# Kernel tuning notes

Hardware: AMD Instinct MI355X
Metric: run time of the kernel (lower is better)

Reference implementation:

```python
import jax, jax.numpy as jnp
import numpy as np

DIM = 384
NUM_HEADS = 12
KERNEL = 3
DILATIONS = (1, 2, 3)
B, H, W = 16, 56, 56


def _unfold(x, k, dil):
    # x: [B, c, H, W] -> [B, c, k*k, H, W]; matches nn.Unfold(k, dilation=dil,
    # padding=dil*(k-1)//2, stride=1) channel ordering [c, kh, kw].
    b, c, h, w = x.shape
    p = dil * (k - 1) // 2
    xp = jnp.pad(x, ((0, 0), (0, 0), (p, p), (p, p)))
    patches = [xp[:, :, i * dil:i * dil + h, j * dil:j * dil + w]
               for i in range(k) for j in range(k)]
    return jnp.stack(patches, axis=2)


def _dilate_attention(q, k, v, head_dim, kernel, dil):
    # q,k,v: [B, c, H, W]
    b, c, h, w = q.shape
    g = c // head_dim           # heads in this dilation branch
    kk = kernel * kernel
    scale = head_dim ** (-0.5)
    qg = q.reshape(b, g, head_dim, h * w)                       # [b,g,d,n]
    ku = _unfold(k, kernel, dil).reshape(b, g, head_dim, kk, h * w)
    vu = _unfold(v, kernel, dil).reshape(b, g, head_dim, kk, h * w)
    attn = jnp.einsum('bgdn,bgdkn->bgnk', qg, ku) * scale       # [b,g,n,kk]
    attn = jax.nn.softmax(attn, axis=-1)
    out = jnp.einsum('bgnk,bgdkn->bgnd', attn, vu)              # [b,g,n,d]
    return out.transpose(0, 2, 1, 3).reshape(b, h, w, c)        # [b,h,w,c]


def setup_inputs() -> dict:
    key = jax.random.key(0)
    kx, kq, kp = jax.random.split(key, 3)
    x = jax.random.normal(kx, (B, H, W, DIM), dtype=jnp.float32)
    w_qkv = jax.random.normal(kq, (3 * DIM, DIM), dtype=jnp.float32) * 0.02
    w_proj = jax.random.normal(kp, (DIM, DIM), dtype=jnp.float32) * 0.02
    b_proj = jnp.zeros((DIM,), dtype=jnp.float32)
    return {"x": x, "w_qkv": w_qkv, "w_proj": w_proj, "b_proj": b_proj}


def reference(x, w_qkv, w_proj, b_proj):
    b, h, w, c = x.shape
    nd = len(DILATIONS)
    cg = c // nd                # channels per dilation branch
    hd = c // NUM_HEADS         # head_dim
    xc = x.transpose(0, 3, 1, 2)                                 # [b,c,h,w]
    qkv = jnp.einsum('bchw,oc->bohw', xc, w_qkv)                 # 1x1 conv, no bias
    qkv = qkv.reshape(b, 3, nd, cg, h, w)
    outs = [_dilate_attention(qkv[:, 0, i], qkv[:, 1, i], qkv[:, 2, i],
                              hd, KERNEL, DILATIONS[i]) for i in range(nd)]
    y = jnp.stack(outs, axis=3).reshape(b, h, w, c)              # [b,h,w, nd*cg]
    return jnp.einsum('bhwc,oc->bhwo', y, w_proj) + b_proj
```

## Files before the change

### kernel.cpp

```cpp
#include <hip/hip_runtime.h>
#include <hip/hip_bf16.h>


#define NTOK 50176
#define ROWQKV 1152
#define CDIM 384

typedef _Float16 half2v __attribute__((ext_vector_type(2)));
typedef _Float16 half8 __attribute__((ext_vector_type(8)));
typedef float floatx4 __attribute__((ext_vector_type(4)));

typedef __attribute__((address_space(1))) const unsigned int GU32;
typedef __attribute__((address_space(3))) unsigned int LU32;

__global__ __launch_bounds__(256) void conv_f32_f16(const float* __restrict__ in,
                                                    _Float16* __restrict__ out, int n4) {
  int i = blockIdx.x * 256 + threadIdx.x;
  const int stride = gridDim.x * 256;
  for (; i < n4; i += stride) {
    float4 v = ((const float4*)in)[i];
    union { _Float16 h[4]; uint2 u; } o;
    o.h[0] = (_Float16)v.x; o.h[1] = (_Float16)v.y;
    o.h[2] = (_Float16)v.z; o.h[3] = (_Float16)v.w;
    ((uint2*)out)[i] = o.u;
  }
}

template <bool HALF_OUT>
__global__ __launch_bounds__(256) void gemm_f16(const _Float16* __restrict__ A,
                                                const _Float16* __restrict__ B,
                                                const float* __restrict__ bias,
                                                void* __restrict__ Cout,
                                                int N, int K) {
  __shared__ _Float16 As[128 * 32];
  __shared__ _Float16 Bs[128 * 32];
  const int tid = threadIdx.x;
  const int lane = tid & 63;
  const int wv = tid >> 6;
  const int wr = wv >> 1, wc = wv & 1;
  const size_t row0 = (size_t)blockIdx.x * 128;
  const int col0 = blockIdx.y * 128;

  const int srow = tid >> 2;
  const int sslot = tid & 3;
  const int gslot = sslot ^ ((srow >> 1) & 3);
  const _Float16* Abase = A + (row0 + srow) * (size_t)K + gslot * 8;
  const _Float16* Bbase = B + ((size_t)(col0 + srow)) * (size_t)K + gslot * 8;
  char* AsB = (char*)As;
  char* BsB = (char*)Bs;

  const int fr = lane & 15;
  const int fq = lane >> 4;
  const int rpos = (fq ^ ((fr >> 1) & 3)) * 8;

  floatx4 acc[4][4];
#pragma unroll
  for (int i = 0; i < 4; ++i)
#pragma unroll
    for (int j = 0; j < 4; ++j) acc[i][j] = (floatx4){0.f, 0.f, 0.f, 0.f};

  for (int k0 = 0; k0 < K; k0 += 32) {
    __builtin_amdgcn_global_load_lds((GU32*)(Abase + k0), (LU32*)(AsB + tid * 16), 16, 0, 0);
    __builtin_amdgcn_global_load_lds((GU32*)(Abase + (size_t)64 * K + k0),
                                     (LU32*)(AsB + tid * 16 + 4096), 16, 0, 0);
    __builtin_amdgcn_global_load_lds((GU32*)(Bbase + k0), (LU32*)(BsB + tid * 16), 16, 0, 0);
    __builtin_amdgcn_global_load_lds((GU32*)(Bbase + (size_t)64 * K + k0),
                                     (LU32*)(BsB + tid * 16 + 4096), 16, 0, 0);
    __syncthreads();
    half8 af[4], bf[4];
#pragma unroll
    for (int f = 0; f < 4; ++f) {
      af[f] = *(const half8*)&As[(wr * 64 + f * 16 + fr) * 32 + rpos];
      bf[f] = *(const half8*)&Bs[(wc * 64 + f * 16 + fr) * 32 + rpos];
    }
#pragma unroll
    for (int i = 0; i < 4; ++i)
#pragma unroll
      for (int j = 0; j < 4; ++j)
        acc[i][j] = __builtin_amdgcn_mfma_f32_16x16x32_f16(af[i], bf[j], acc[i][j], 0, 0, 0);
    __syncthreads();
  }

  const int crow = wr * 64 + (lane >> 4) * 4;
  const int ccol = wc * 64 + (lane & 15);
#pragma unroll
  for (int fm = 0; fm < 4; ++fm) {
#pragma unroll
    for (int fn = 0; fn < 4; ++fn) {
      const size_t r0 = (row0 + crow + fm * 16) * (size_t)N + col0 + ccol + fn * 16;
      if (HALF_OUT) {
        _Float16* C = (_Float16*)Cout;
#pragma unroll
        for (int j = 0; j < 4; ++j) C[r0 + (size_t)j * N] = (_Float16)acc[fm][fn][j];
      } else {
        float* C = (float*)Cout;
        const float bz = bias[col0 + ccol + fn * 16];
#pragma unroll
        for (int j = 0; j < 4; ++j) C[r0 + (size_t)j * N] = acc[fm][fn][j] + bz;
      }
    }
  }
}

__global__ __launch_bounds__(256) void attn_kernel(const _Float16* __restrict__ qkv,
                                                   _Float16* __restrict__ y) {
  const int idx = blockIdx.x * 256 + threadIdx.x;
  const int head = idx % 12;
  const int token = idx / 12;
  const int branch = head >> 2;
  const int dil = branch + 1;
  const int cbase = branch * 128 + (head & 3) * 32;
  const int xx = token % 56;
  const int yy = (token / 56) % 56;
  const int bimg = token / 3136;
  const float scale = 0.17677669529663687f;

  const _Float16* qp = qkv + (size_t)token * ROWQKV + cbase;
  half2v qh[16];
  *(half8*)&qh[0] = *(const half8*)(qp);
  *(half8*)&qh[4] = *(const half8*)(qp + 8);
  *(half8*)&qh[8] = *(const half8*)(qp + 16);
  *(half8*)&qh[12] = *(const half8*)(qp + 24);

  const size_t nbase = (size_t)bimg * 3136;

  float l[9];
#pragma unroll
  for (int j = 0; j < 9; ++j) {
    const int ny = yy + (j / 3 - 1) * dil;
    const int nx = xx + (j % 3 - 1) * dil;
    float d = 0.f;
    if ((unsigned)ny < 56u && (unsigned)nx < 56u) {
      const _Float16* kp = qkv + (nbase + ny * 56 + nx) * ROWQKV + 384 + cbase;
      half2v kh[16];
      *(half8*)&kh[0] = *(const half8*)(kp);
      *(half8*)&kh[4] = *(const half8*)(kp + 8);
      *(half8*)&kh[8] = *(const half8*)(kp + 16);
      *(half8*)&kh[12] = *(const half8*)(kp + 24);
#if __has_builtin(__builtin_amdgcn_fdot2)
#pragma unroll
      for (int c = 0; c < 16; ++c) d = __builtin_amdgcn_fdot2(qh[c], kh[c], d, false);
#else
#pragma unroll
      for (int c = 0; c < 16; ++c)
        d += (float)qh[c][0] * (float)kh[c][0] + (float)qh[c][1] * (float)kh[c][1];
#endif
    }
    l[j] = d * scale;
  }

  float m = l[0];
#pragma unroll
  for (int j = 1; j < 9; ++j) m = fmaxf(m, l[j]);
  float s = 0.f;
#pragma unroll
  for (int j = 0; j < 9; ++j) { l[j] = expf(l[j] - m); s += l[j]; }
  const float rs = 1.f / s;

  float out[32];
#pragma unroll
  for (int c = 0; c < 32; ++c) out[c] = 0.f;
#pragma unroll
  for (int j = 0; j < 9; ++j) {
    const int ny = yy + (j / 3 - 1) * dil;
    const int nx = xx + (j % 3 - 1) * dil;
    if ((unsigned)ny < 56u && (unsigned)nx < 56u) {
      const _Float16* vp = qkv + (nbase + ny * 56 + nx) * ROWQKV + 768 + cbase;
      half8 vh[4];
      vh[0] = *(const half8*)(vp);
      vh[1] = *(const half8*)(vp + 8);
      vh[2] = *(const half8*)(vp + 16);
      vh[3] = *(const half8*)(vp + 24);
      const float p = l[j];
#pragma unroll
      for (int g = 0; g < 4; ++g)
#pragma unroll
        for (int e = 0; e < 8; ++e) out[g * 8 + e] = fmaf(p, (float)vh[g][e], out[g * 8 + e]);
    }
  }

  _Float16* yp = y + (size_t)token * CDIM + cbase;
  half8 oh[4];
#pragma unroll
  for (int g = 0; g < 4; ++g) {
#pragma unroll
    for (int e = 0; e < 8; ++e) oh[g][e] = (_Float16)(out[g * 8 + e] * rs);
    *(half8*)(yp + g * 8) = oh[g];
  }
}

extern "C" void kernel_launch(void* const* d_in, const int* in_sizes, int n_in,
                              void* d_out, int out_size, void* d_ws, size_t ws_size,
                              hipStream_t stream) {
  const float* x = (const float*)d_in[0];
  const float* w_qkv = (const float*)d_in[1];
  const float* w_proj = (const float*)d_in[2];
  const float* b_proj = (const float*)d_in[3];
  float* out = (float*)d_out;

  _Float16* xh = (_Float16*)d_ws;
  _Float16* wqh = xh + (size_t)NTOK * CDIM;
  _Float16* wph = wqh + (size_t)ROWQKV * CDIM;
  _Float16* qkvh = wph + (size_t)CDIM * CDIM;
  _Float16* yh = qkvh + (size_t)NTOK * ROWQKV;

  conv_f32_f16<<<2048, 256, 0, stream>>>(x, xh, NTOK * CDIM / 4);
  conv_f32_f16<<<64, 256, 0, stream>>>(w_qkv, wqh, ROWQKV * CDIM / 4);
  conv_f32_f16<<<64, 256, 0, stream>>>(w_proj, wph, CDIM * CDIM / 4);

  gemm_f16<true><<<dim3(NTOK / 128, ROWQKV / 128), 256, 0, stream>>>(
      xh, wqh, nullptr, qkvh, ROWQKV, CDIM);

  attn_kernel<<<(NTOK * 12) / 256, 256, 0, stream>>>(qkvh, yh);

  gemm_f16<false><<<dim3(NTOK / 128, CDIM / 128), 256, 0, stream>>>(
      yh, wph, b_proj, out, CDIM, CDIM);
}
```

Measured before the change: 208.8 us.

## Fuse x fp32-to-fp16 conversion into QKV GEMM and double-buffer LDS tiles

The QKV GEMM now reads fp32 activations directly, converts them to fp16 in registers and writes them swizzled into LDS. This removes the separate conversion kernel and its fp16 copy of x. Both GEMMs also gain double-buffered LDS tiles, so the next K-slice is prefetched while MFMAs run on the current one, with one barrier per iteration instead of two. The cost is twice the LDS footprint, which may lower occupancy, and fp32 A is re-read once per column block (9 times for QKV), doubling A traffic compared with fp16.

```diff
diff --git a/kernel.cpp b/kernel.cpp
--- a/kernel.cpp
+++ b/kernel.cpp
@@ -26,28 +26,76 @@
   }
 }
 
-template <bool HALF_OUT>
-__global__ __launch_bounds__(256) void gemm_f16(const _Float16* __restrict__ A,
-                                                const _Float16* __restrict__ B,
-                                                const float* __restrict__ bias,
-                                                void* __restrict__ Cout,
-                                                int N, int K) {
-  __shared__ _Float16 As[128 * 32];
-  __shared__ _Float16 Bs[128 * 32];
+template <bool CONV_A, bool HALF_OUT>
+__global__ __launch_bounds__(256) void gemm2(const void* __restrict__ Aptr,
+                                             const _Float16* __restrict__ B,
+                                             const float* __restrict__ bias,
+                                             void* __restrict__ Cout,
+                                             int N, int K) {
+  __shared__ _Float16 As[2][128 * 32];
+  __shared__ _Float16 Bs[2][128 * 32];
   const int tid = threadIdx.x;
   const int lane = tid & 63;
   const int wv = tid >> 6;
   const int wr = wv >> 1, wc = wv & 1;
   const size_t row0 = (size_t)blockIdx.x * 128;
   const int col0 = blockIdx.y * 128;
+  const int NT = K / 32;
 
   const int srow = tid >> 2;
-  const int sslot = tid & 3;
-  const int gslot = sslot ^ ((srow >> 1) & 3);
-  const _Float16* Abase = A + (row0 + srow) * (size_t)K + gslot * 8;
+  const int gslot = (tid & 3) ^ ((srow >> 1) & 3);
   const _Float16* Bbase = B + ((size_t)(col0 + srow)) * (size_t)K + gslot * 8;
+  char* BsB = (char*)Bs;
+
+  const int ar = tid >> 1, ah = tid & 1;
+  const float* Af32 = (const float*)Aptr + (row0 + ar) * (size_t)K + ah * 16;
+  const int asw0 = (ah * 2) ^ ((ar >> 1) & 3);
+  const int asw1 = (ah * 2 + 1) ^ ((ar >> 1) & 3);
+  const _Float16* Abase16 = (const _Float16*)Aptr + (row0 + srow) * (size_t)K + gslot * 8;
   char* AsB = (char*)As;
-  char* BsB = (char*)Bs;
+
+  float4 av[4];
+  auto loadA = [&](int k0) {
+    if constexpr (CONV_A) {
+      av[0] = *(const float4*)(Af32 + k0);
+      av[1] = *(const float4*)(Af32 + k0 + 4);
+      av[2] = *(const float4*)(Af32 + k0 + 8);
+      av[3] = *(const float4*)(Af32 + k0 + 12);
+    } else {
+      __builtin_amdgcn_global_load_lds((GU32*)(Abase16 + k0), (LU32*)(AsB + tid * 16), 16, 0, 0);
+      __builtin_amdgcn_global_load_lds((GU32*)(Abase16 + (size_t)64 * K + k0),
+                                       (LU32*)(AsB + tid * 16 + 4096), 16, 0, 0);
+    }
+  };
+  auto loadA2 = [&](int k0, int buf) {
+    if constexpr (!CONV_A) {
+      __builtin_amdgcn_global_load_lds((GU32*)(Abase16 + k0),
+                                       (LU32*)(AsB + buf * 8192 + tid * 16), 16, 0, 0);
+      __builtin_amdgcn_global_load_lds((GU32*)(Abase16 + (size_t)64 * K + k0),
+                                       (LU32*)(AsB + buf * 8192 + tid * 16 + 4096), 16, 0, 0);
+    }
+  };
+  auto writeA = [&](int buf) {
+    if constexpr (CONV_A) {
+      half8 lo, hi;
+      lo[0] = (_Float16)av[0].x; lo[1] = (_Float16)av[0].y;
+      lo[2] = (_Float16)av[0].z; lo[3] = (_Float16)av[0].w;
+      lo[4] = (_Float16)av[1].x; lo[5] = (_Float16)av[1].y;
+      lo[6] = (_Float16)av[1].z; lo[7] = (_Float16)av[1].w;
+      hi[0] = (_Float16)av[2].x; hi[1] = (_Float16)av[2].y;
+      hi[2] = (_Float16)av[2].z; hi[3] = (_Float16)av[2].w;
+      hi[4] = (_Float16)av[3].x; hi[5] = (_Float16)av[3].y;
+      hi[6] = (_Float16)av[3].z; hi[7] = (_Float16)av[3].w;
+      *(half8*)&As[buf][ar * 32 + asw0 * 8] = lo;
+      *(half8*)&As[buf][ar * 32 + asw1 * 8] = hi;
+    }
+  };
+  auto stageB = [&](int k0, int buf) {
+    __builtin_amdgcn_global_load_lds((GU32*)(Bbase + k0),
+                                     (LU32*)(BsB + buf * 8192 + tid * 16), 16, 0, 0);
+    __builtin_amdgcn_global_load_lds((GU32*)(Bbase + (size_t)64 * K + k0),
+                                     (LU32*)(BsB + buf * 8192 + tid * 16 + 4096), 16, 0, 0);
+  };
 
   const int fr = lane & 15;
   const int fq = lane >> 4;
@@ -59,26 +107,31 @@
 #pragma unroll
     for (int j = 0; j < 4; ++j) acc[i][j] = (floatx4){0.f, 0.f, 0.f, 0.f};
 
-  for (int k0 = 0; k0 < K; k0 += 32) {
-    __builtin_amdgcn_global_load_lds((GU32*)(Abase + k0), (LU32*)(AsB + tid * 16), 16, 0, 0);
-    __builtin_amdgcn_global_load_lds((GU32*)(Abase + (size_t)64 * K + k0),
-                                     (LU32*)(AsB + tid * 16 + 4096), 16, 0, 0);
-    __builtin_amdgcn_global_load_lds((GU32*)(Bbase + k0), (LU32*)(BsB + tid * 16), 16, 0, 0);
-    __builtin_amdgcn_global_load_lds((GU32*)(Bbase + (size_t)64 * K + k0),
-                                     (LU32*)(BsB + tid * 16 + 4096), 16, 0, 0);
-    __syncthreads();
+  if constexpr (CONV_A) { loadA(0); writeA(0); } else { loadA2(0, 0); }
+  stageB(0, 0);
+  __syncthreads();
+
+  int cur = 0;
+  for (int t = 0; t < NT; ++t) {
+    const int k1 = (t + 1) * 32;
+    if (t + 1 < NT) {
+      if constexpr (CONV_A) loadA(k1); else loadA2(k1, cur ^ 1);
+      stageB(k1, cur ^ 1);
+    }
     half8 af[4], bf[4];
 #pragma unroll
     for (int f = 0; f < 4; ++f) {
-      af[f] = *(const half8*)&As[(wr * 64 + f * 16 + fr) * 32 + rpos];
-      bf[f] = *(const half8*)&Bs[(wc * 64 + f * 16 + fr) * 32 + rpos];
+      af[f] = *(const half8*)&As[cur][(wr * 64 + f * 16 + fr) * 32 + rpos];
+      bf[f] = *(const half8*)&Bs[cur][(wc * 64 + f * 16 + fr) * 32 + rpos];
     }
 #pragma unroll
     for (int i = 0; i < 4; ++i)
 #pragma unroll
       for (int j = 0; j < 4; ++j)
         acc[i][j] = __builtin_amdgcn_mfma_f32_16x16x32_f16(af[i], bf[j], acc[i][j], 0, 0, 0);
+    if (t + 1 < NT) writeA(cur ^ 1);
     __syncthreads();
+    cur ^= 1;
   }
 
   const int crow = wr * 64 + (lane >> 4) * 4;
@@ -198,21 +251,19 @@
   const float* b_proj = (const float*)d_in[3];
   float* out = (float*)d_out;
 
-  _Float16* xh = (_Float16*)d_ws;
-  _Float16* wqh = xh + (size_t)NTOK * CDIM;
+  _Float16* wqh = (_Float16*)d_ws;
   _Float16* wph = wqh + (size_t)ROWQKV * CDIM;
   _Float16* qkvh = wph + (size_t)CDIM * CDIM;
   _Float16* yh = qkvh + (size_t)NTOK * ROWQKV;
 
-  conv_f32_f16<<<2048, 256, 0, stream>>>(x, xh, NTOK * CDIM / 4);
   conv_f32_f16<<<64, 256, 0, stream>>>(w_qkv, wqh, ROWQKV * CDIM / 4);
   conv_f32_f16<<<64, 256, 0, stream>>>(w_proj, wph, CDIM * CDIM / 4);
 
-  gemm_f16<true><<<dim3(NTOK / 128, ROWQKV / 128), 256, 0, stream>>>(
-      xh, wqh, nullptr, qkvh, ROWQKV, CDIM);
+  gemm2<true, true><<<dim3(NTOK / 128, ROWQKV / 128), 256, 0, stream>>>(
+      x, wqh, nullptr, qkvh, ROWQKV, CDIM);
 
   attn_kernel<<<(NTOK * 12) / 256, 256, 0, stream>>>(qkvh, yh);
 
-  gemm_f16<false><<<dim3(NTOK / 128, CDIM / 128), 256, 0, stream>>>(
+  gemm2<false, false><<<dim3(NTOK / 128, CDIM / 128), 256, 0, stream>>>(
       yh, wph, b_proj, out, CDIM, CDIM);
 }
```

Measured after the change: 217.3 us. 4.1% more time.

## Double-buffer GEMM LDS tiles, remap blocks for XCD locality, merge conversion kernels

Applied to the files above, without the earlier changes.

The GEMM now uses two LDS buffers and issues the next K-tile's global-to-LDS loads before computing on the current tile, so memory latency can overlap the MFMA work. Blocks are launched on a 1D grid and remapped so that consecutive logical tiles land on the same XCD (index modulo 8), which is meant to improve L2 reuse of the A rows. The three fp32-to-fp16 conversion launches are merged into one kernel to save launch overhead. In exchange, LDS use per block doubles, which may lower occupancy. The remap also assumes the grid size is a multiple of 8.

```diff
diff --git a/kernel.cpp b/kernel.cpp
--- a/kernel.cpp
+++ b/kernel.cpp
@@ -13,42 +13,72 @@
 typedef __attribute__((address_space(1))) const unsigned int GU32;
 typedef __attribute__((address_space(3))) unsigned int LU32;
 
-__global__ __launch_bounds__(256) void conv_f32_f16(const float* __restrict__ in,
-                                                    _Float16* __restrict__ out, int n4) {
+#define N_X4 (NTOK * CDIM / 4)
+#define N_Q4 (ROWQKV * CDIM / 4)
+#define N_P4 (CDIM * CDIM / 4)
+
+__global__ __launch_bounds__(256) void conv_all(const float* __restrict__ x,
+                                                const float* __restrict__ wq,
+                                                const float* __restrict__ wp,
+                                                _Float16* __restrict__ xh,
+                                                _Float16* __restrict__ wqh,
+                                                _Float16* __restrict__ wph) {
+  const int total = N_X4 + N_Q4 + N_P4;
   int i = blockIdx.x * 256 + threadIdx.x;
   const int stride = gridDim.x * 256;
-  for (; i < n4; i += stride) {
-    float4 v = ((const float4*)in)[i];
+  for (; i < total; i += stride) {
+    const float* src;
+    _Float16* dst;
+    int k;
+    if (i < N_X4) { src = x; dst = xh; k = i; }
+    else if (i < N_X4 + N_Q4) { src = wq; dst = wqh; k = i - N_X4; }
+    else { src = wp; dst = wph; k = i - N_X4 - N_Q4; }
+    float4 v = ((const float4*)src)[k];
     union { _Float16 h[4]; uint2 u; } o;
     o.h[0] = (_Float16)v.x; o.h[1] = (_Float16)v.y;
     o.h[2] = (_Float16)v.z; o.h[3] = (_Float16)v.w;
-    ((uint2*)out)[i] = o.u;
+    ((uint2*)dst)[k] = o.u;
   }
 }
 
 template <bool HALF_OUT>
-__global__ __launch_bounds__(256) void gemm_f16(const _Float16* __restrict__ A,
-                                                const _Float16* __restrict__ B,
-                                                const float* __restrict__ bias,
-                                                void* __restrict__ Cout,
-                                                int N, int K) {
-  __shared__ _Float16 As[128 * 32];
-  __shared__ _Float16 Bs[128 * 32];
+__global__ __launch_bounds__(256) void gemm3(const _Float16* __restrict__ A,
+                                             const _Float16* __restrict__ B,
+                                             const float* __restrict__ bias,
+                                             void* __restrict__ Cout,
+                                             int N, int K) {
+  __shared__ _Float16 As[2][128 * 32];
+  __shared__ _Float16 Bs[2][128 * 32];
   const int tid = threadIdx.x;
   const int lane = tid & 63;
   const int wv = tid >> 6;
   const int wr = wv >> 1, wc = wv & 1;
-  const size_t row0 = (size_t)blockIdx.x * 128;
-  const int col0 = blockIdx.y * 128;
+
+  const int nN = N >> 7;
+  const int p = blockIdx.x;
+  const int l = (p & 7) * (gridDim.x >> 3) + (p >> 3);
+  const size_t row0 = (size_t)(l / nN) * 128;
+  const int col0 = (l % nN) * 128;
+  const int NT = K / 32;
 
   const int srow = tid >> 2;
-  const int sslot = tid & 3;
-  const int gslot = sslot ^ ((srow >> 1) & 3);
+  const int gslot = (tid & 3) ^ ((srow >> 1) & 3);
   const _Float16* Abase = A + (row0 + srow) * (size_t)K + gslot * 8;
   const _Float16* Bbase = B + ((size_t)(col0 + srow)) * (size_t)K + gslot * 8;
   char* AsB = (char*)As;
   char* BsB = (char*)Bs;
 
+  auto stage = [&](int k0, int buf) {
+    __builtin_amdgcn_global_load_lds((GU32*)(Abase + k0),
+                                     (LU32*)(AsB + buf * 8192 + tid * 16), 16, 0, 0);
+    __builtin_amdgcn_global_load_lds((GU32*)(Abase + (size_t)64 * K + k0),
+                                     (LU32*)(AsB + buf * 8192 + tid * 16 + 4096), 16, 0, 0);
+    __builtin_amdgcn_global_load_lds((GU32*)(Bbase + k0),
+                                     (LU32*)(BsB + buf * 8192 + tid * 16), 16, 0, 0);
+    __builtin_amdgcn_global_load_lds((GU32*)(Bbase + (size_t)64 * K + k0),
+                                     (LU32*)(BsB + buf * 8192 + tid * 16 + 4096), 16, 0, 0);
+  };
+
   const int fr = lane & 15;
   const int fq = lane >> 4;
   const int rpos = (fq ^ ((fr >> 1) & 3)) * 8;
@@ -59,19 +89,17 @@
 #pragma unroll
     for (int j = 0; j < 4; ++j) acc[i][j] = (floatx4){0.f, 0.f, 0.f, 0.f};
 
-  for (int k0 = 0; k0 < K; k0 += 32) {
-    __builtin_amdgcn_global_load_lds((GU32*)(Abase + k0), (LU32*)(AsB + tid * 16), 16, 0, 0);
-    __builtin_amdgcn_global_load_lds((GU32*)(Abase + (size_t)64 * K + k0),
-                                     (LU32*)(AsB + tid * 16 + 4096), 16, 0, 0);
-    __builtin_amdgcn_global_load_lds((GU32*)(Bbase + k0), (LU32*)(BsB + tid * 16), 16, 0, 0);
-    __builtin_amdgcn_global_load_lds((GU32*)(Bbase + (size_t)64 * K + k0),
-                                     (LU32*)(BsB + tid * 16 + 4096), 16, 0, 0);
-    __syncthreads();
+  stage(0, 0);
+  __syncthreads();
+
+  int cur = 0;
+  for (int t = 0; t < NT; ++t) {
+    if (t + 1 < NT) stage((t + 1) * 32, cur ^ 1);
     half8 af[4], bf[4];
 #pragma unroll
     for (int f = 0; f < 4; ++f) {
-      af[f] = *(const half8*)&As[(wr * 64 + f * 16 + fr) * 32 + rpos];
-      bf[f] = *(const half8*)&Bs[(wc * 64 + f * 16 + fr) * 32 + rpos];
+      af[f] = *(const half8*)&As[cur][(wr * 64 + f * 16 + fr) * 32 + rpos];
+      bf[f] = *(const half8*)&Bs[cur][(wc * 64 + f * 16 + fr) * 32 + rpos];
     }
 #pragma unroll
     for (int i = 0; i < 4; ++i)
@@ -79,6 +107,7 @@
       for (int j = 0; j < 4; ++j)
         acc[i][j] = __builtin_amdgcn_mfma_f32_16x16x32_f16(af[i], bf[j], acc[i][j], 0, 0, 0);
     __syncthreads();
+    cur ^= 1;
   }
 
   const int crow = wr * 64 + (lane >> 4) * 4;
@@ -204,15 +233,13 @@
   _Float16* qkvh = wph + (size_t)CDIM * CDIM;
   _Float16* yh = qkvh + (size_t)NTOK * ROWQKV;
 
-  conv_f32_f16<<<2048, 256, 0, stream>>>(x, xh, NTOK * CDIM / 4);
-  conv_f32_f16<<<64, 256, 0, stream>>>(w_qkv, wqh, ROWQKV * CDIM / 4);
-  conv_f32_f16<<<64, 256, 0, stream>>>(w_proj, wph, CDIM * CDIM / 4);
-
-  gemm_f16<true><<<dim3(NTOK / 128, ROWQKV / 128), 256, 0, stream>>>(
+  conv_all<<<2048, 256, 0, stream>>>(x, w_qkv, w_proj, xh, wqh, wph);
+
+  gemm3<true><<<(NTOK / 128) * (ROWQKV / 128), 256, 0, stream>>>(
       xh, wqh, nullptr, qkvh, ROWQKV, CDIM);
 
   attn_kernel<<<(NTOK * 12) / 256, 256, 0, stream>>>(qkvh, yh);
 
-  gemm_f16<false><<<dim3(NTOK / 128, CDIM / 128), 256, 0, stream>>>(
+  gemm3<false><<<(NTOK / 128) * (CDIM / 128), 256, 0, stream>>>(
       yh, wph, b_proj, out, CDIM, CDIM);
 }
```

Result: faster. 187.9 us (-10.0%).
